# Kernel optimization log

Measured on AMD Instinct MI355X. Metric: run time of the kernel, lower is better.

Reference implementation:

```python
import jax, jax.numpy as jnp
import numpy as np

WH, WW = 7, 7
N = WH * WW
H = 16          # num_heads
D = 32          # head_dim
NW = 64         # num windows per image (mask.shape[0])


def _relative_position_index(wh, ww):
    coords = np.stack(np.meshgrid(np.arange(wh), np.arange(ww), indexing='ij'))  # (2, wh, ww)
    cf = coords.reshape(2, -1)                                                   # (2, N)
    rel = cf[:, :, None] - cf[:, None, :]                                        # (2, N, N)
    rel = rel.transpose(1, 2, 0).copy()
    rel[:, :, 0] += wh - 1
    rel[:, :, 1] += ww - 1
    rel[:, :, 0] *= 2 * ww - 1
    return rel.sum(-1)  # (N, N) int

REL_IDX = jnp.asarray(_relative_position_index(WH, WW))


def setup_inputs() -> dict:
    key = jax.random.key(0)
    ks = jax.random.split(key, 5)
    B_ = 2048
    dim = H * D
    x = jax.random.normal(ks[0], (B_, N, dim), dtype=jnp.float32)
    mask = jnp.zeros((NW, N, N), dtype=jnp.float32)
    rpb_table = jax.random.normal(ks[1], ((2 * WH - 1) * (2 * WW - 1), H), dtype=jnp.float32) * 0.02
    qkv_w = jax.random.normal(ks[2], (3 * dim, dim), dtype=jnp.float32) * (dim ** -0.5)
    qkv_b = jnp.zeros((3 * dim,), dtype=jnp.float32)
    proj_w = jax.random.normal(ks[3], (dim, dim), dtype=jnp.float32) * (dim ** -0.5)
    proj_b = jnp.zeros((dim,), dtype=jnp.float32)
    return {"x": x, "mask": mask, "rpb_table": rpb_table,
            "qkv_w": qkv_w, "qkv_b": qkv_b, "proj_w": proj_w, "proj_b": proj_b}


def reference(x, mask, rpb_table, qkv_w, qkv_b, proj_w, proj_b):
    B_, n, C = x.shape
    scale = D ** -0.5
    # qkv projection (torch Linear: x @ W^T + b)
    qkv = (x @ qkv_w.T + qkv_b).reshape(B_, n, 3, H, D)
    q = qkv[:, :, 0].transpose(0, 2, 1, 3) * scale  # (B_, H, N, D)
    k = qkv[:, :, 1].transpose(0, 2, 1, 3)
    v = qkv[:, :, 2].transpose(0, 2, 1, 3)
    attn = jnp.einsum('bhnd,bhmd->bhnm', q, k)      # (B_, H, N, N)
    # relative position bias: gather (N*N,) rows from table -> (N, N, H) -> (H, N, N)
    bias = rpb_table[REL_IDX.reshape(-1)].reshape(n, n, H).transpose(2, 0, 1)
    attn = attn + bias[None]
    # shifted-window mask add: (B, nW, H, N, N) + (1, nW, 1, N, N)
    nW = mask.shape[0]
    attn = attn.reshape(B_ // nW, nW, H, n, n) + mask[None, :, None]
    attn = attn.reshape(B_, H, n, n)
    attn = jax.nn.softmax(attn, axis=-1)
    out = jnp.einsum('bhnm,bhmd->bhnd', attn, v)    # (B_, H, N, D)
    out = out.transpose(0, 2, 1, 3).reshape(B_, n, H * D)
    return out @ proj_w.T + proj_b
```

## Files before the change

### kernel.cpp

```cpp
#include <hip/hip_runtime.h>

typedef _Float16 f16;
typedef _Float16 f16x8 __attribute__((ext_vector_type(8)));
typedef _Float16 f16x4 __attribute__((ext_vector_type(4)));
typedef float f32x4 __attribute__((ext_vector_type(4)));

#define NTOK 49
#define NH 16
#define HD 32
#define DIM 512
#define NWIN 64
#define NB 2048
#define MTOT (NB*NTOK)
#define SCALE 0.17677669529663687f
#define VTS 56

__device__ __forceinline__ void gload_lds16(const f16* g, f16* l) {
    __builtin_amdgcn_global_load_lds((const __attribute__((address_space(1))) void*)g,
                                     (__attribute__((address_space(3))) void*)l, 16, 0, 0);
}

__global__ __launch_bounds__(256) void cvt_f32_f16(const float* __restrict__ s,
                                                   f16* __restrict__ d, int n4) {
    int i = blockIdx.x * 256 + threadIdx.x;
    int st = gridDim.x * 256;
    for (; i < n4; i += st) {
        float4 v = ((const float4*)s)[i];
        f16x4 o = { (f16)v.x, (f16)v.y, (f16)v.z, (f16)v.w };
        *(f16x4*)(d + (size_t)i * 4) = o;
    }
}

__global__ __launch_bounds__(256) void build_comb2(const float* __restrict__ rpb,
                                                   const float* __restrict__ mask,
                                                   float* __restrict__ comb2) {
    int idx = blockIdx.x * 256 + threadIdx.x;
    int r4   = idx & 3;
    int tj   = (idx >> 2) & 3;
    int ti   = (idx >> 4) & 3;
    int lane = (idx >> 6) & 63;
    int wh   = idx >> 12;
    int h = wh & 15, w = wh >> 4;
    int g = lane >> 4, c16 = lane & 15;
    int row = ti * 16 + g * 4 + r4;
    int col = tj * 16 + c16;
    float v = 0.f;
    if (row < NTOK && col < NTOK) {
        int ri = row / 7, ci = row - ri * 7;
        int rj = col / 7, cj = col - rj * 7;
        int rel = (ri - rj + 6) * 13 + (ci - cj + 6);
        v = rpb[rel * NH + h] + mask[(w * NTOK + row) * NTOK + col];
    }
    comb2[idx] = v;
}

template<int MODE>
__global__ __launch_bounds__(256) void gemm_kernel(const f16* __restrict__ A,
                                                   const f16* __restrict__ Bw,
                                                   const float* __restrict__ bias,
                                                   f16* __restrict__ qo,
                                                   f16* __restrict__ ko,
                                                   f16* __restrict__ vto,
                                                   float* __restrict__ outp) {
    __shared__ __align__(16) f16 As[128][64];
    __shared__ __align__(16) f16 Bs[128][64];

    const int tid = threadIdx.x;
    const int lane = tid & 63;
    const int wv = tid >> 6;
    const int wr = wv >> 1, wc = wv & 1;
    const int g = lane >> 4, c16 = lane & 15;
    const int m0 = blockIdx.x * 128;
    const int n0 = blockIdx.y * 128;

    const int sr = lane >> 3;
    const int sc = (lane & 7) * 8;
    const f16* gA = A + (size_t)(m0 + wv * 32 + sr) * DIM + sc;
    const f16* gB = Bw + (size_t)(n0 + wv * 32 + sr) * DIM + sc;
    f16* lA = &As[wv * 32][0];
    f16* lB = &Bs[wv * 32][0];

    f32x4 acc[4][4];
#pragma unroll
    for (int i = 0; i < 4; ++i)
#pragma unroll
        for (int j = 0; j < 4; ++j)
            acc[i][j] = (f32x4){0.f, 0.f, 0.f, 0.f};

    const int KS = DIM / 64;
    for (int ks = 0; ks < KS; ++ks) {
        const int k0 = ks * 64;
        __syncthreads();
#pragma unroll
        for (int i = 0; i < 4; ++i) {
            gload_lds16(gA + (size_t)(i * 8) * DIM + k0, lA + i * 8 * 64);
            gload_lds16(gB + (size_t)(i * 8) * DIM + k0, lB + i * 8 * 64);
        }
        __syncthreads();
#pragma unroll
        for (int kk = 0; kk < 2; ++kk) {
            f16x8 af[4], bf[4];
#pragma unroll
            for (int t = 0; t < 4; ++t)
                af[t] = *(const f16x8*)&As[wr * 64 + t * 16 + c16][kk * 32 + g * 8];
#pragma unroll
            for (int t = 0; t < 4; ++t)
                bf[t] = *(const f16x8*)&Bs[wc * 64 + t * 16 + c16][kk * 32 + g * 8];
#pragma unroll
            for (int i = 0; i < 4; ++i)
#pragma unroll
                for (int j = 0; j < 4; ++j)
                    acc[i][j] = __builtin_amdgcn_mfma_f32_16x16x32_f16(af[i], bf[j], acc[i][j], 0, 0, 0);
        }
    }

#pragma unroll
    for (int i = 0; i < 4; ++i)
#pragma unroll
        for (int r = 0; r < 4; ++r) {
            int m = m0 + wr * 64 + i * 16 + g * 4 + r;
            int b = 0, t = 0;
            if (MODE == 0) { b = m / NTOK; t = m - b * NTOK; }
#pragma unroll
            for (int j = 0; j < 4; ++j) {
                int n = n0 + wc * 64 + j * 16 + c16;
                float v = acc[i][j][r] + bias[n];
                if (MODE == 0) {
                    int s = n >> 9;
                    int hh = (n >> 5) & 15;
                    int d = n & 31;
                    int bh = b * NH + hh;
                    if (s == 0)      qo[((size_t)bh * NTOK + t) * HD + d] = (f16)(v * SCALE);
                    else if (s == 1) ko[((size_t)bh * NTOK + t) * HD + d] = (f16)v;
                    else             vto[((size_t)bh * HD + d) * VTS + t] = (f16)v;
                } else {
                    outp[(size_t)m * DIM + n] = v;
                }
            }
        }
}

__global__ __launch_bounds__(256) void attn_kernel(const f16* __restrict__ qw,
                                                   const f16* __restrict__ kw,
                                                   const f16* __restrict__ vt,
                                                   const float* __restrict__ comb2,
                                                   f16* __restrict__ aout) {
    __shared__ __align__(16) f16 Ps[4][64][72];

    const int wv = threadIdx.x >> 6;
    const int l = threadIdx.x & 63;
    const int bid = blockIdx.x * 4 + wv;
    const int b = bid >> 4, h = bid & 15;
    const int w = b & (NWIN - 1);
    const int g = l >> 4, c16 = l & 15;
    const size_t qkbase = (size_t)bid * (NTOK * HD);
    const size_t vbase = (size_t)bid * (HD * VTS);

    const f16x8 z8 = {};

    f16x8 qf[4], kf[4];
#pragma unroll
    for (int t = 0; t < 4; ++t) {
        int row = t * 16 + c16;
        f16x8 q = z8, k = z8;
        if (row < NTOK) {
            q = *(const f16x8*)(qw + qkbase + row * HD + g * 8);
            k = *(const f16x8*)(kw + qkbase + row * HD + g * 8);
        }
        qf[t] = q; kf[t] = k;
    }

    const float* cb = comb2 + (((size_t)(w * NH + h) * 64 + l) << 6);
    f32x4 S[4][4];
#pragma unroll
    for (int i = 0; i < 4; ++i)
#pragma unroll
        for (int j = 0; j < 4; ++j)
            S[i][j] = *(const f32x4*)(cb + (i * 4 + j) * 4);
#pragma unroll
    for (int i = 0; i < 4; ++i)
#pragma unroll
        for (int j = 0; j < 4; ++j)
            S[i][j] = __builtin_amdgcn_mfma_f32_16x16x32_f16(qf[i], kf[j], S[i][j], 0, 0, 0);

#pragma unroll
    for (int ti = 0; ti < 4; ++ti)
#pragma unroll
        for (int r = 0; r < 4; ++r) {
            int row = ti * 16 + g * 4 + r;
            float v0 = S[ti][0][r], v1 = S[ti][1][r], v2 = S[ti][2][r];
            float v3 = (c16 == 0) ? S[ti][3][r] : -1e30f;
            float mx = fmaxf(fmaxf(v0, v1), fmaxf(v2, v3));
#pragma unroll
            for (int mk = 1; mk < 16; mk <<= 1) mx = fmaxf(mx, __shfl_xor(mx, mk, 64));
            float p0 = __expf(v0 - mx), p1 = __expf(v1 - mx), p2 = __expf(v2 - mx);
            float p3 = (c16 == 0) ? __expf(v3 - mx) : 0.f;
            float sm = p0 + p1 + p2 + p3;
#pragma unroll
            for (int mk = 1; mk < 16; mk <<= 1) sm += __shfl_xor(sm, mk, 64);
            float inv = 1.f / sm;
            Ps[wv][row][c16]      = (f16)(p0 * inv);
            Ps[wv][row][16 + c16] = (f16)(p1 * inv);
            Ps[wv][row][32 + c16] = (f16)(p2 * inv);
            Ps[wv][row][48 + c16] = (f16)(p3 * inv);
        }
    __syncthreads();

    f32x4 O[4][2];
    const f32x4 zf = (f32x4){0.f, 0.f, 0.f, 0.f};
#pragma unroll
    for (int i = 0; i < 4; ++i) { O[i][0] = zf; O[i][1] = zf; }
#pragma unroll
    for (int c = 0; c < 2; ++c) {
        f16x8 pf[4], vf[2];
#pragma unroll
        for (int ti = 0; ti < 4; ++ti)
            pf[ti] = *(const f16x8*)&Ps[wv][ti * 16 + c16][c * 32 + g * 8];
        int tcol = c * 32 + g * 8;
#pragma unroll
        for (int td = 0; td < 2; ++td) {
            f16x8 vv = z8;
            if (tcol < VTS)
                vv = *(const f16x8*)(vt + vbase + (size_t)(td * 16 + c16) * VTS + tcol);
            vf[td] = vv;
        }
#pragma unroll
        for (int ti = 0; ti < 4; ++ti)
#pragma unroll
            for (int td = 0; td < 2; ++td)
                O[ti][td] = __builtin_amdgcn_mfma_f32_16x16x32_f16(pf[ti], vf[td], O[ti][td], 0, 0, 0);
    }

#pragma unroll
    for (int ti = 0; ti < 4; ++ti)
#pragma unroll
        for (int r = 0; r < 4; ++r) {
            int row = ti * 16 + g * 4 + r;
            if (row < NTOK) {
                size_t ob = ((size_t)(b * NTOK + row)) * DIM + h * HD;
                aout[ob + c16]      = (f16)O[ti][0][r];
                aout[ob + 16 + c16] = (f16)O[ti][1][r];
            }
        }
}

extern "C" void kernel_launch(void* const* d_in, const int* in_sizes, int n_in,
                              void* d_out, int out_size, void* d_ws, size_t ws_size,
                              hipStream_t stream) {
    const float* x      = (const float*)d_in[0];
    const float* mask   = (const float*)d_in[1];
    const float* rpb    = (const float*)d_in[2];
    const float* qkv_w  = (const float*)d_in[3];
    const float* qkv_b  = (const float*)d_in[4];
    const float* proj_w = (const float*)d_in[5];
    const float* proj_b = (const float*)d_in[6];
    float* out = (float*)d_out;

    char* ws = (char*)d_ws;
    size_t o = 0;
    f16* x16   = (f16*)(ws + o); o += (size_t)MTOT * DIM * 2;
    f16* w16   = (f16*)(ws + o); o += (size_t)1536 * 512 * 2;
    f16* pw16  = (f16*)(ws + o); o += (size_t)512 * 512 * 2;
    f16* qws   = (f16*)(ws + o); o += (size_t)NB * NH * NTOK * HD * 2;
    f16* kws   = (f16*)(ws + o); o += (size_t)NB * NH * NTOK * HD * 2;
    f16* vtws  = (f16*)(ws + o); o += (size_t)NB * NH * HD * VTS * 2;
    float* cb2 = (float*)(ws + o);
    f16* aout = x16;

    cvt_f32_f16<<<dim3(2048), dim3(256), 0, stream>>>(x, x16, MTOT * DIM / 4);
    cvt_f32_f16<<<dim3(768), dim3(256), 0, stream>>>(qkv_w, w16, 1536 * 512 / 4);
    cvt_f32_f16<<<dim3(256), dim3(256), 0, stream>>>(proj_w, pw16, 512 * 512 / 4);

    build_comb2<<<dim3(16384), dim3(256), 0, stream>>>(rpb, mask, cb2);

    gemm_kernel<0><<<dim3(MTOT / 128, 1536 / 128), dim3(256), 0, stream>>>(
        x16, w16, qkv_b, qws, kws, vtws, nullptr);

    attn_kernel<<<dim3(NB * NH / 4), dim3(256), 0, stream>>>(qws, kws, vtws, cb2, aout);

    gemm_kernel<1><<<dim3(MTOT / 128, 512 / 128), dim3(256), 0, stream>>>(
        aout, pw16, proj_b, nullptr, nullptr, nullptr, out);
}
```

Baseline: 650.9 us.

## Double-buffer GEMM LDS tiles, swizzle LDS layout, remap blocks across XCDs

Measured after the change: 695.8 us. 1.07x slower.

```diff
diff --git a/kernel.cpp b/kernel.cpp
--- a/kernel.cpp
+++ b/kernel.cpp
@@ -54,7 +54,7 @@
     comb2[idx] = v;
 }
 
-template<int MODE>
+template<int MODE, int NT>
 __global__ __launch_bounds__(256) void gemm_kernel(const f16* __restrict__ A,
                                                    const f16* __restrict__ Bw,
                                                    const float* __restrict__ bias,
@@ -62,23 +62,25 @@
                                                    f16* __restrict__ ko,
                                                    f16* __restrict__ vto,
                                                    float* __restrict__ outp) {
-    __shared__ __align__(16) f16 As[128][64];
-    __shared__ __align__(16) f16 Bs[128][64];
+    __shared__ __align__(16) f16 As[2][128][64];
+    __shared__ __align__(16) f16 Bs[2][128][64];
 
     const int tid = threadIdx.x;
     const int lane = tid & 63;
     const int wv = tid >> 6;
     const int wr = wv >> 1, wc = wv & 1;
     const int g = lane >> 4, c16 = lane & 15;
-    const int m0 = blockIdx.x * 128;
-    const int n0 = blockIdx.y * 128;
-
-    const int sr = lane >> 3;
-    const int sc = (lane & 7) * 8;
-    const f16* gA = A + (size_t)(m0 + wv * 32 + sr) * DIM + sc;
-    const f16* gB = Bw + (size_t)(n0 + wv * 32 + sr) * DIM + sc;
-    f16* lA = &As[wv * 32][0];
-    f16* lB = &Bs[wv * 32][0];
+
+    const int nblk = gridDim.x;
+    const int f = blockIdx.x;
+    const int work = (f & 7) * (nblk >> 3) + (f >> 3);
+    const int m0 = (work / NT) * 128;
+    const int n0 = (work % NT) * 128;
+
+    const int sr8 = lane >> 3;
+    const int scs = ((lane & 7) ^ sr8) * 8;
+    const f16* gA = A + (size_t)(m0 + wv * 32 + sr8) * DIM + scs;
+    const f16* gB = Bw + (size_t)(n0 + wv * 32 + sr8) * DIM + scs;
 
     f32x4 acc[4][4];
 #pragma unroll
@@ -87,31 +89,42 @@
         for (int j = 0; j < 4; ++j)
             acc[i][j] = (f32x4){0.f, 0.f, 0.f, 0.f};
 
+#pragma unroll
+    for (int i = 0; i < 4; ++i) {
+        gload_lds16(gA + (size_t)(i * 8) * DIM, &As[0][wv * 32 + i * 8][0]);
+        gload_lds16(gB + (size_t)(i * 8) * DIM, &Bs[0][wv * 32 + i * 8][0]);
+    }
+
     const int KS = DIM / 64;
+    int cur = 0;
     for (int ks = 0; ks < KS; ++ks) {
-        const int k0 = ks * 64;
         __syncthreads();
-#pragma unroll
-        for (int i = 0; i < 4; ++i) {
-            gload_lds16(gA + (size_t)(i * 8) * DIM + k0, lA + i * 8 * 64);
-            gload_lds16(gB + (size_t)(i * 8) * DIM + k0, lB + i * 8 * 64);
-        }
-        __syncthreads();
+        if (ks + 1 < KS) {
+            const int k0 = (ks + 1) * 64;
+#pragma unroll
+            for (int i = 0; i < 4; ++i) {
+                gload_lds16(gA + (size_t)(i * 8) * DIM + k0, &As[cur ^ 1][wv * 32 + i * 8][0]);
+                gload_lds16(gB + (size_t)(i * 8) * DIM + k0, &Bs[cur ^ 1][wv * 32 + i * 8][0]);
+            }
+        }
 #pragma unroll
         for (int kk = 0; kk < 2; ++kk) {
             f16x8 af[4], bf[4];
 #pragma unroll
             for (int t = 0; t < 4; ++t)
-                af[t] = *(const f16x8*)&As[wr * 64 + t * 16 + c16][kk * 32 + g * 8];
+                af[t] = *(const f16x8*)&As[cur][wr * 64 + t * 16 + c16][((kk * 4 + g) ^ (c16 & 7)) * 8];
 #pragma unroll
             for (int t = 0; t < 4; ++t)
-                bf[t] = *(const f16x8*)&Bs[wc * 64 + t * 16 + c16][kk * 32 + g * 8];
+                bf[t] = *(const f16x8*)&Bs[cur][wc * 64 + t * 16 + c16][((kk * 4 + g) ^ (c16 & 7)) * 8];
+            __builtin_amdgcn_s_setprio(1);
 #pragma unroll
             for (int i = 0; i < 4; ++i)
 #pragma unroll
                 for (int j = 0; j < 4; ++j)
                     acc[i][j] = __builtin_amdgcn_mfma_f32_16x16x32_f16(af[i], bf[j], acc[i][j], 0, 0, 0);
-        }
+            __builtin_amdgcn_s_setprio(0);
+        }
+        cur ^= 1;
     }
 
 #pragma unroll
@@ -149,7 +162,9 @@
 
     const int wv = threadIdx.x >> 6;
     const int l = threadIdx.x & 63;
-    const int bid = blockIdx.x * 4 + wv;
+    const int f = blockIdx.x;
+    const int work = (f & 7) * (gridDim.x >> 3) + (f >> 3);
+    const int bid = work * 4 + wv;
     const int b = bid >> 4, h = bid & 15;
     const int w = b & (NWIN - 1);
     const int g = l >> 4, c16 = l & 15;
@@ -273,11 +288,11 @@
 
     build_comb2<<<dim3(16384), dim3(256), 0, stream>>>(rpb, mask, cb2);
 
-    gemm_kernel<0><<<dim3(MTOT / 128, 1536 / 128), dim3(256), 0, stream>>>(
+    gemm_kernel<0, 12><<<dim3((MTOT / 128) * 12), dim3(256), 0, stream>>>(
         x16, w16, qkv_b, qws, kws, vtws, nullptr);
 
     attn_kernel<<<dim3(NB * NH / 4), dim3(256), 0, stream>>>(qws, kws, vtws, cb2, aout);
 
-    gemm_kernel<1><<<dim3(MTOT / 128, 512 / 128), dim3(256), 0, stream>>>(
+    gemm_kernel<1, 4><<<dim3((MTOT / 128) * 4), dim3(256), 0, stream>>>(
         aout, pw16, proj_b, nullptr, nullptr, nullptr, out);
 }
```
